# Kernel tuning notes

Measured on AMD Instinct MI355X. Metric: run time of the kernel, lower is better.

Reference implementation:

```python
import jax, jax.numpy as jnp
import numpy as np

N, C, K, H, F, O = 100000, 64, 32, 4, 256, 64
HD = C // H
EPS = 1e-5


def _bn(x, gamma, beta):
    # BatchNorm1d in training mode: biased batch statistics over the voxel dim
    mu = x.mean(axis=0)
    var = x.var(axis=0)
    return (x - mu) * jax.lax.rsqrt(var + EPS) * gamma + beta


def setup_inputs() -> dict:
    key = jax.random.key(0)
    ks = jax.random.split(key, 24)
    s = 0.05
    inp = {
        "voxel_features": jax.random.normal(ks[0], (N, C), jnp.float32),
        "voxel_coords": jax.random.uniform(ks[1], (N, 3), jnp.float32) * 70.0,
        "key_indices": jax.random.randint(ks[2], (N, K), 0, N, jnp.int32),
        "key_mask": jax.random.randint(ks[3], (N, K), 0, 2, jnp.int32).astype(bool).at[:, 0].set(False),
        # MultiheadAttention in/out projections
        "wq": jax.random.normal(ks[4], (C, C), jnp.float32) * s,
        "bq": jnp.zeros((C,), jnp.float32),
        "wk": jax.random.normal(ks[5], (C, C), jnp.float32) * s,
        "bk": jnp.zeros((C,), jnp.float32),
        "wv": jax.random.normal(ks[6], (C, C), jnp.float32) * s,
        "bv": jnp.zeros((C,), jnp.float32),
        "wo": jax.random.normal(ks[7], (C, C), jnp.float32) * s,
        "bo": jnp.zeros((C,), jnp.float32),
        # positional embedding projections (q: Linear(3,C); k: Conv1d(3,C,1) == Linear)
        "q_pos_w": jax.random.normal(ks[8], (C, 3), jnp.float32) * s,
        "q_pos_b": jnp.zeros((C,), jnp.float32),
        "k_pos_w": jax.random.normal(ks[9], (C, 3), jnp.float32) * s,
        "k_pos_b": jnp.zeros((C,), jnp.float32),
        # norm1 / norm2 BatchNorm params
        "g1": jnp.ones((C,), jnp.float32), "b1": jnp.zeros((C,), jnp.float32),
        "g2": jnp.ones((C,), jnp.float32), "b2": jnp.zeros((C,), jnp.float32),
        # FFN
        "lin1_w": jax.random.normal(ks[10], (F, C), jnp.float32) * s,
        "lin1_b": jnp.zeros((F,), jnp.float32),
        "lin2_w": jax.random.normal(ks[11], (C, F), jnp.float32) * s,
        "lin2_b": jnp.zeros((C,), jnp.float32),
        # output layer: Linear + BN + ReLU
        "out_w": jax.random.normal(ks[12], (O, C), jnp.float32) * s,
        "out_b": jnp.zeros((O,), jnp.float32),
        "g3": jnp.ones((O,), jnp.float32), "b3": jnp.zeros((O,), jnp.float32),
    }
    return inp


def reference(voxel_features, voxel_coords, key_indices, key_mask,
              wq, bq, wk, bk, wv, bv, wo, bo,
              q_pos_w, q_pos_b, k_pos_w, k_pos_b,
              g1, b1, g2, b2,
              lin1_w, lin1_b, lin2_w, lin2_b,
              out_w, out_b, g3, b3):
    # gather neighbor features / coords: [N, K, C] and [N, K, 3]
    key_feat = voxel_features[key_indices]
    key_coords = voxel_coords[key_indices] - voxel_coords[:, None, :]  # relative coords

    # positional embeddings
    key_feat = key_feat + jax.nn.relu(jnp.einsum("nkt,ct->nkc", key_coords, k_pos_w) + k_pos_b)
    query = voxel_features + jax.nn.relu(voxel_coords @ q_pos_w.T + q_pos_b)

    # multihead attention: one query per voxel over K gathered keys
    q = (query @ wq.T + bq).reshape(N, H, HD)
    k = (key_feat @ wk.T + bk).reshape(N, K, H, HD)
    v = (key_feat @ wv.T + bv).reshape(N, K, H, HD)
    scores = jnp.einsum("nhd,nkhd->nhk", q, k) / np.sqrt(HD).astype(np.float32)
    scores = jnp.where(key_mask[:, None, :], -jnp.inf, scores)
    attn = jax.nn.softmax(scores, axis=-1)  # [N, H, K]
    ctx = jnp.einsum("nhk,nkhd->nhd", attn, v).reshape(N, C)
    attend = ctx @ wo.T + bo

    # residual + norm1 (dropout = 0)
    x = _bn(voxel_features + attend, g1, b1)
    # FFN + residual + norm2
    ff = jax.nn.relu(x @ lin1_w.T + lin1_b) @ lin2_w.T + lin2_b
    x = _bn(x + ff, g2, b2)
    # output layer: Linear -> BN -> ReLU
    out = jax.nn.relu(_bn(x @ out_w.T + out_b, g3, b3))
    return out
```

## Files before the change

kernel.cpp:

```cpp
#include <hip/hip_runtime.h>
#include <hip/hip_bf16.h>

#define NV 100000
#define EPSB 1e-5f

typedef unsigned short u16;
typedef unsigned int u32;
typedef _Float16 hv2 __attribute__((ext_vector_type(2)));
typedef _Float16 h8  __attribute__((ext_vector_type(8)));
typedef float f32x4  __attribute__((ext_vector_type(4)));

__device__ __forceinline__ u32 pkh(float x, float y) {
  auto h = __builtin_amdgcn_cvt_pkrtz(x, y);
  union { decltype(h) v; u32 u; } c; c.v = h; return c.u;
}
__device__ __forceinline__ float fdot2(u32 w, u32 x, float acc) {
#if __has_builtin(__builtin_amdgcn_fdot2)
  union { u32 u; hv2 h; } a, b; a.u = w; b.u = x;
  return __builtin_amdgcn_fdot2(a.h, b.h, acc, false);
#else
  union { u32 u; hv2 h; } a, b; a.u = w; b.u = x;
  return acc + (float)a.h.x*(float)b.h.x + (float)a.h.y*(float)b.h.y;
#endif
}
__device__ __forceinline__ u32 bcastu(u32 v, int l) {
  return (u32)__builtin_amdgcn_readlane((int)v, l);
}
__device__ __forceinline__ hv2 as_hv(u32 u) {
  union { u32 u; hv2 h; } c; c.u = u; return c.h;
}
__device__ __forceinline__ u32 as_u32h(hv2 h) {
  union { hv2 h; u32 u; } c; c.h = h; return c.u;
}
__device__ __forceinline__ hv2 hmax2v(hv2 a, hv2 b) {
#if __has_builtin(__builtin_elementwise_max)
  return __builtin_elementwise_max(a, b);
#else
  hv2 r; r.x = a.x > b.x ? a.x : b.x; r.y = a.y > b.y ? a.y : b.y; return r;
#endif
}
__device__ __forceinline__ hv2 hfma2v(hv2 a, hv2 b, hv2 c) {
#if __has_builtin(__builtin_elementwise_fma)
  return __builtin_elementwise_fma(a, b, c);
#else
  return a * b + c;
#endif
}
__device__ __forceinline__ u16 f2h(float x) { return (u16)(pkh(x, x) & 0xffffu); }
__device__ __forceinline__ float h2f(u16 u) {
  union { u16 u; _Float16 h; } c; c.u = u; return (float)c.h;
}
__device__ __forceinline__ f32x4 mfma16(h8 a, h8 b, f32x4 c) {
  return __builtin_amdgcn_mfma_f32_16x16x32_f16(a, b, c, 0, 0, 0);
}

__global__ void k0_detect(const u32* __restrict__ km, int* __restrict__ flag) {
  int bad = 0;
  for (int i = threadIdx.x; i < 4096; i += 256) {
    u32 v = km[i];
    bad |= (v != 0u && v != 1u && v != 0x3F800000u) ? 1 : 0;
  }
  unsigned long long m = __ballot(bad != 0);
  __shared__ int sbad[4];
  if ((threadIdx.x & 63) == 0) sbad[threadIdx.x >> 6] = (m != 0ull);
  __syncthreads();
  if (threadIdx.x == 0) flag[0] = !(sbad[0] | sbad[1] | sbad[2] | sbad[3]);
}

__global__ __launch_bounds__(256) void k_prep(
    const float* __restrict__ vf, const float* __restrict__ coords,
    const float* __restrict__ kpw, u32* __restrict__ VP)
{
  const int t = blockIdx.x*256 + threadIdx.x;
  const int cp = t & 31;
  const float wa0 = kpw[(2*cp)*3],   wa1 = kpw[(2*cp)*3+1],   wa2 = kpw[(2*cp)*3+2];
  const float wb0 = kpw[(2*cp+1)*3], wb1 = kpw[(2*cp+1)*3+1], wb2 = kpw[(2*cp+1)*3+2];
  for (int e = t; e < NV*32; e += 524288) {
    const int m = e >> 5;
    const float2 v2 = *(const float2*)&vf[(u32)m*64u + 2u*(u32)cp];
    const float c0 = coords[m*3], c1 = coords[m*3+1], c2 = coords[m*3+2];
    const float P0 = fmaf(wa0, c0, fmaf(wa1, c1, wa2*c2));
    const float P1 = fmaf(wb0, c0, fmaf(wb1, c1, wb2*c2));
    uint2 o; o.x = pkh(v2.x, v2.y); o.y = pkh(P0, P1);
    *(uint2*)&VP[(u32)e*2u] = o;
  }
}

__global__ __launch_bounds__(512, 4) void k1_attn(
    const float* __restrict__ vf, const float* __restrict__ coords,
    const int* __restrict__ kidx, const void* __restrict__ kmaskv,
    const int* __restrict__ mflag, const u32* __restrict__ VP,
    const float* __restrict__ wq, const float* __restrict__ bq,
    const float* __restrict__ wk,
    const float* __restrict__ wv, const float* __restrict__ bv,
    const float* __restrict__ wo, const float* __restrict__ bo,
    const float* __restrict__ qpw, const float* __restrict__ qpb,
    const float* __restrict__ kpb,
    float* __restrict__ x1pre, float* __restrict__ stats)
{
  extern __shared__ char smem[];
  uint2* WQP2 = (uint2*)smem;
  uint2* WKP2 = WQP2 + 1024;
  uint2* WVP2 = WKP2 + 1024;
  uint2* WOP2 = WVP2 + 1024;
  const int tid = threadIdx.x, wid = tid >> 6, lane = tid & 63;

  for (int t = tid; t < 1024; t += 512) {
    int cp = t >> 6, i = t & 63;
    uint2 v;
    v.x = pkh(wq[i*64 + 2*cp],      wq[i*64 + 2*cp + 1]);
    v.y = pkh(wq[i*64 + 2*cp + 32], wq[i*64 + 2*cp + 33]);
    WQP2[t] = v;
    int lo = (cp < 8) ? cp : cp + 8, hi = lo + 8;
    v.x = pkh(wk[2*lo*64 + i], wk[(2*lo+1)*64 + i]);
    v.y = pkh(wk[2*hi*64 + i], wk[(2*hi+1)*64 + i]);
    WKP2[t] = v;
    v.x = pkh(wv[i*64 + 2*cp],      wv[i*64 + 2*cp + 1]);
    v.y = pkh(wv[i*64 + 2*cp + 32], wv[i*64 + 2*cp + 33]);
    WVP2[t] = v;
    v.x = pkh(wo[i*64 + 2*cp],      wo[i*64 + 2*cp + 1]);
    v.y = pkh(wo[i*64 + 2*cp + 32], wo[i*64 + 2*cp + 33]);
    WOP2[t] = v;
  }
  __syncthreads();

  u32* wbase = (u32*)(smem + 32768) + wid * 1360;
  u32*   KFp  = wbase;
  uint2* QKH2 = (uint2*)(wbase + 1088);
  uint2* API2 = QKH2;
  u32*   SPP  = wbase + 1216;

  const int cl = lane & 31, kh = lane >> 5, hp = lane >> 5, hh = lane >> 4;
  const int ca = 2*cl;
  const float qp0 = qpw[lane*3], qp1 = qpw[lane*3+1], qp2 = qpw[lane*3+2], qpbl = qpb[lane];
  const hv2 kpbp = as_hv(pkh(kpb[ca], kpb[ca+1]));
  const hv2 z2 = (hv2)(_Float16)0;
  const float bql = bq[lane], bvl = bv[lane], bol = bo[lane];
  const int mode4 = mflag[0];
  const u32* km32 = (const u32*)kmaskv;
  const unsigned char* km8 = (const unsigned char*)kmaskv;
  float ssum = 0.f, ssq = 0.f;

  for (int n = blockIdx.x*8 + wid; n < NV; n += 4096) {
    const float cn0 = coords[n*3], cn1 = coords[n*3+1], cn2 = coords[n*3+2];
    u32 mk;
    if (mode4) mk = (km32[n*32 + cl] != 0u);
    else       mk = (km8[n*32 + cl]  != 0u);
    const float vfl = vf[(u32)n*64u + (u32)lane];
    const uint2 wn = *(const uint2*)&VP[(u32)n*64u + (u32)ca];
    const hv2 pnp = as_hv(wn.y) - kpbp;

    union { int4 v[4]; int s[16]; } iu;
    {
      const int4* kp4 = (const int4*)(kidx + (u32)n*32u + (u32)(kh*16));
      iu.v[0] = kp4[0]; iu.v[1] = kp4[1]; iu.v[2] = kp4[2]; iu.v[3] = kp4[3];
    }

    #pragma unroll
    for (int b = 0; b < 2; ++b) {
      uint2 g[8];
      #pragma unroll
      for (int k = 0; k < 8; ++k) {
        const u32 off = ((u32)iu.s[b*8+k] << 6) + (u32)ca;
        g[k] = *(const uint2*)&VP[off];
      }
      #pragma unroll
      for (int k = 0; k < 8; ++k) {
        hv2 pe = hmax2v(as_hv(g[k].y) - pnp, z2);
        KFp[(kh*16 + b*8 + k)*34 + cl] = as_u32h(as_hv(g[k].x) + pe);
      }
    }

    float query = vfl + fmaxf(fmaf(qp0,cn0,fmaf(qp1,cn1,fmaf(qp2,cn2,qpbl))), 0.f);
    const u32 qpk = pkh(query, __shfl_down(query, 1));

    float qa0 = bql, qa1 = 0.f;
    #pragma unroll
    for (int cp = 0; cp < 16; ++cp) {
      uint2 w = WQP2[cp*64 + lane];
      qa0 = fdot2(w.x, bcastu(qpk, 2*cp     ), qa0);
      qa1 = fdot2(w.y, bcastu(qpk, 2*cp + 32), qa1);
    }
    const float qacc = (qa0 + qa1) * 0.25f;
    const u32 qpk2 = pkh(qacc, __shfl_down(qacc, 1));

    float qkh0=0.f, qkh1=0.f, qkh2=0.f, qkh3=0.f;
    #pragma unroll
    for (int p = 0; p < 8; ++p) {
      uint2 wA = WKP2[ p    *64 + lane];
      uint2 wB = WKP2[(p+8) *64 + lane];
      qkh0 = fdot2(wA.x, bcastu(qpk2, 2*p     ), qkh0);
      qkh1 = fdot2(wA.y, bcastu(qpk2, 2*p + 16), qkh1);
      qkh2 = fdot2(wB.x, bcastu(qpk2, 2*p + 32), qkh2);
      qkh3 = fdot2(wB.y, bcastu(qpk2, 2*p + 48), qkh3);
    }
    {
      float t0 = __shfl_down(qkh0, 1), t1 = __shfl_down(qkh1, 1);
      float t2 = __shfl_down(qkh2, 1), t3 = __shfl_down(qkh3, 1);
      if ((lane & 1) == 0) {
        int j = lane >> 1;
        uint2 v0; v0.x = pkh(qkh0, t0); v0.y = pkh(qkh1, t1);
        uint2 v1; v1.x = pkh(qkh2, t2); v1.y = pkh(qkh3, t3);
        QKH2[j]      = v0;
        QKH2[32 + j] = v1;
      }
    }

    float s00=0.f, s01=0.f, s10=0.f, s11=0.f;
    {
      const u32* kfrow = KFp + cl*34;
      const uint2* qrow = QKH2 + hp*32;
      #pragma unroll
      for (int c2 = 0; c2 < 16; ++c2) {
        uint2 kf = *(const uint2*)(kfrow + 2*c2);
        uint2 q0 = qrow[2*c2];
        uint2 q1 = qrow[2*c2 + 1];
        s00 = fdot2(kf.x, q0.x, s00);
        s10 = fdot2(kf.x, q0.y, s10);
        s01 = fdot2(kf.y, q1.x, s01);
        s11 = fdot2(kf.y, q1.y, s11);
      }
    }
    float sc0 = s00 + s01, sc1 = s10 + s11;
    if (mk) { sc0 = -1e30f; sc1 = -1e30f; }

    float m0 = sc0, m1 = sc1;
    #pragma unroll
    for (int off = 16; off; off >>= 1) {
      m0 = fmaxf(m0, __shfl_xor(m0, off));
      m1 = fmaxf(m1, __shfl_xor(m1, off));
    }
    float p0 = __expf(sc0 - m0), p1 = __expf(sc1 - m1);
    float s0 = p0, s1 = p1;
    #pragma unroll
    for (int off = 16; off; off >>= 1) {
      s0 += __shfl_xor(s0, off);
      s1 += __shfl_xor(s1, off);
    }
    const float a0 = p0 / s0, a1 = p1 / s1;

    {
      uint2 ap; ap.x = pkh(a0, a0); ap.y = pkh(a1, a1);
      API2[lane] = ap;
    }

    const int j = lane & 31;
    const int ab = hp << 5;
    hv2 accA = z2, accB = z2;
    #pragma unroll
    for (int k2 = 0; k2 < 32; ++k2) {
      hv2 kf = as_hv(KFp[k2*34 + j]);
      uint2 ap = API2[ab + k2];
      accA = hfma2v(kf, as_hv(ap.x), accA);
      accB = hfma2v(kf, as_hv(ap.y), accB);
    }
    {
      const int sj = (j & 15)*2 + (j >> 4);
      SPP[(2*hp  )*34 + sj] = as_u32h(accA);
      SPP[(2*hp+1)*34 + sj] = as_u32h(accB);
    }

    float ca0 = bvl, ca1 = 0.f;
    {
      const u32* sprow = SPP + hh*34;
      #pragma unroll
      for (int cp = 0; cp < 16; ++cp) {
        uint2 s = *(const uint2*)(sprow + 2*cp);
        uint2 w = WVP2[cp*64 + lane];
        ca0 = fdot2(w.x, s.x, ca0);
        ca1 = fdot2(w.y, s.y, ca1);
      }
    }
    const float cacc = ca0 + ca1;
    const u32 cpk = pkh(cacc, __shfl_down(cacc, 1));

    float oa0 = bol, oa1 = 0.f;
    #pragma unroll
    for (int cp = 0; cp < 16; ++cp) {
      uint2 w = WOP2[cp*64 + lane];
      oa0 = fdot2(w.x, bcastu(cpk, 2*cp     ), oa0);
      oa1 = fdot2(w.y, bcastu(cpk, 2*cp + 32), oa1);
    }
    const float aacc = oa0 + oa1;

    float x1 = vfl + aacc;
    x1pre[(u32)n*64u + (u32)lane] = x1;
    ssum += x1; ssq = fmaf(x1, x1, ssq);
  }

  __syncthreads();
  float* red = (float*)smem;
  red[wid*64 + lane] = ssum;
  red[512 + wid*64 + lane] = ssq;
  __syncthreads();
  if (wid == 0) {
    float t1 = 0.f, t2 = 0.f;
    #pragma unroll
    for (int w = 0; w < 8; ++w) { t1 += red[w*64+lane]; t2 += red[512+w*64+lane]; }
    atomicAdd(&stats[lane], t1);
    atomicAdd(&stats[64+lane], t2);
  }
}

__global__ __launch_bounds__(512) void k3_mfma(
    const float* __restrict__ x1pre, float* __restrict__ stats,
    const float* __restrict__ g1, const float* __restrict__ b1,
    const float* __restrict__ l1w, const float* __restrict__ l1b,
    const float* __restrict__ l2w, const float* __restrict__ l2b,
    float* __restrict__ x2pre)
{
  extern __shared__ char smem[];
  u32*   W1B  = (u32*)smem;
  u32*   W2B  = W1B + 8192;
  u16*   XA   = (u16*)(W2B + 8192);
  u16*   H    = XA + 4608;
  float* l1bs = (float*)(H + 16896);
  float* l2bs = l1bs + 256;
  float* scb  = l2bs + 64;
  float* shb  = scb + 64;
  float* red  = shb + 64;
  const int tid = threadIdx.x, wid = tid >> 6, lane = tid & 63;

  for (int e = tid; e < 8192; e += 512) {
    int j2 = e & 3, col = (e>>2) & 15, g = (e>>6) & 3, kk = (e>>8) & 1, n = e >> 9;
    int f = 16*n + col, k = kk*32 + g*8 + 2*j2;
    W1B[e] = pkh(l1w[f*64 + k], l1w[f*64 + k + 1]);
  }
  for (int e = tid; e < 8192; e += 512) {
    int j2 = e & 3, col = (e>>2) & 15, g = (e>>6) & 3, kk = (e>>8) & 7, n = e >> 11;
    int c = 16*n + col, k = kk*32 + g*8 + 2*j2;
    W2B[e] = pkh(l2w[c*256 + k], l2w[c*256 + k + 1]);
  }
  if (tid < 256) l1bs[tid] = l1b[tid];
  if (tid < 64)  l2bs[tid] = l2b[tid];
  if (tid < 64) {
    float mean = stats[tid] * (1.f/NV);
    float var  = stats[64+tid] * (1.f/NV) - mean*mean;
    float sc = rsqrtf(var + EPSB) * g1[tid];
    scb[tid] = sc;
    shb[tid] = b1[tid] - mean * sc;
  }
  if (tid < 128) red[tid] = 0.f;

  const int m  = wid & 3;
  const int wh = wid >> 2;
  const int lg = lane >> 4, ll = lane & 15;
  float ss0 = 0.f, sq0 = 0.f, ss1 = 0.f, sq1 = 0.f;

  for (int tile = blockIdx.x; tile < 1563; tile += 256) {
    const int base = tile * 64;
    __syncthreads();
    {
      int row = tid >> 3, cq = (tid & 7) * 8;
      int srow = base + row; if (srow >= NV) srow = NV - 1;
      const float* src = x1pre + (size_t)srow*64 + cq;
      u32* dst = (u32*)XA + row*36 + (tid & 7)*4;
      #pragma unroll
      for (int q = 0; q < 4; ++q) {
        float v0 = src[2*q]   * scb[cq+2*q]   + shb[cq+2*q];
        float v1 = src[2*q+1] * scb[cq+2*q+1] + shb[cq+2*q+1];
        dst[q] = pkh(v0, v1);
      }
    }
    __syncthreads();
    {
      const u16* arow = XA + (16*m + ll)*72 + lg*8;
      h8 a0 = *(const h8*)(arow);
      h8 a1 = *(const h8*)(arow + 32);
      #pragma unroll
      for (int nn = 0; nn < 8; ++nn) {
        int n = 8*wh + nn;
        const u32* bb = W1B + (n*8 + lg)*64 + ll*4;
        h8 b0 = *(const h8*)(bb);
        h8 b1v = *(const h8*)(bb + 256);
        f32x4 acc = {0.f, 0.f, 0.f, 0.f};
        acc = mfma16(a0, b0, acc);
        acc = mfma16(a1, b1v, acc);
        float bias = l1bs[16*n + ll];
        u16* hw = H + (16*m + lg*4)*264 + 16*n + ll;
        #pragma unroll
        for (int r = 0; r < 4; ++r)
          hw[r*264] = f2h(fmaxf(acc[r] + bias, 0.f));
      }
    }
    __syncthreads();
    {
      const u16* arow = H + (16*m + ll)*264 + lg*8;
      h8 a[8];
      #pragma unroll
      for (int kk = 0; kk < 8; ++kk) a[kk] = *(const h8*)(arow + kk*32);
      #pragma unroll
      for (int nn = 0; nn < 2; ++nn) {
        int n = 2*wh + nn;
        const u32* bb = W2B + (n*32 + lg)*64 + ll*4;
        f32x4 acA = {0.f,0.f,0.f,0.f}, acB = {0.f,0.f,0.f,0.f};
        #pragma unroll
        for (int kk = 0; kk < 8; kk += 2) {
          h8 b0 = *(const h8*)(bb + kk*256);
          h8 b1v = *(const h8*)(bb + (kk+1)*256);
          acA = mfma16(a[kk],   b0,  acA);
          acB = mfma16(a[kk+1], b1v, acB);
        }
        const int col = 16*n + ll;
        const float bias = l2bs[col];
        const u16* xr = XA + (16*m + lg*4)*72 + col;
        const int vox0 = base + 16*m + lg*4;
        float ss = 0.f, sq = 0.f;
        #pragma unroll
        for (int r = 0; r < 4; ++r) {
          int vox = vox0 + r;
          if (vox < NV) {
            float y = acA[r] + acB[r] + bias + h2f(xr[r*72]);
            x2pre[(size_t)vox*64 + col] = y;
            ss += y; sq = fmaf(y, y, sq);
          }
        }
        if (nn == 0) { ss0 += ss; sq0 += sq; } else { ss1 += ss; sq1 += sq; }
      }
    }
  }

  __syncthreads();
  const int c2a = 16*(2*wh)     + ll;
  const int c2b = 16*(2*wh + 1) + ll;
  atomicAdd(&red[c2a], ss0);
  atomicAdd(&red[64 + c2a], sq0);
  atomicAdd(&red[c2b], ss1);
  atomicAdd(&red[64 + c2b], sq1);
  __syncthreads();
  if (tid < 64) {
    atomicAdd(&stats[128+tid], red[tid]);
    atomicAdd(&stats[192+tid], red[64+tid]);
  }
}

__global__ __launch_bounds__(256) void k4_out(
    const float* __restrict__ x2pre, float* __restrict__ stats,
    const float* __restrict__ g2, const float* __restrict__ b2,
    const float* __restrict__ outw, const float* __restrict__ outb,
    float* __restrict__ outpre)
{
  extern __shared__ char smem[];
  u32* WTP = (u32*)smem;
  const int tid = threadIdx.x, wid = tid >> 6, lane = tid & 63;
  for (int t = tid; t < 2048; t += 256) {
    int cp = t >> 6, o = t & 63;
    WTP[t] = pkh(outw[o*64 + 2*cp], outw[o*64 + 2*cp + 1]);
  }
  __syncthreads();

  const float mean = stats[128+lane] * (1.f/NV);
  const float var  = stats[192+lane] * (1.f/NV) - mean*mean;
  const float sc   = rsqrtf(var + EPSB) * g2[lane];
  const float sh   = b2[lane] - mean * sc;
  const float obl  = outb[lane];
  float ssum = 0.f, ssq = 0.f;

  const int stride = gridDim.x << 4;
  for (int n0 = blockIdx.x*16 + wid*4; n0 < NV; n0 += stride) {
    float xa = x2pre[(size_t) n0   *64+lane] * sc + sh;
    float xb = x2pre[(size_t)(n0+1)*64+lane] * sc + sh;
    float xc = x2pre[(size_t)(n0+2)*64+lane] * sc + sh;
    float xd = x2pre[(size_t)(n0+3)*64+lane] * sc + sh;
    const u32 xpa = pkh(xa, __shfl_down(xa,1));
    const u32 xpb = pkh(xb, __shfl_down(xb,1));
    const u32 xpc = pkh(xc, __shfl_down(xc,1));
    const u32 xpd = pkh(xd, __shfl_down(xd,1));
    float a0 = obl, a1 = obl, a2 = obl, a3 = obl;
    #pragma unroll 8
    for (int cp = 0; cp < 32; ++cp) {
      u32 w = WTP[cp*64 + lane];
      a0 = fdot2(w, bcastu(xpa, 2*cp), a0);
      a1 = fdot2(w, bcastu(xpb, 2*cp), a1);
      a2 = fdot2(w, bcastu(xpc, 2*cp), a2);
      a3 = fdot2(w, bcastu(xpd, 2*cp), a3);
    }
    outpre[(size_t) n0   *64+lane] = a0;
    outpre[(size_t)(n0+1)*64+lane] = a1;
    outpre[(size_t)(n0+2)*64+lane] = a2;
    outpre[(size_t)(n0+3)*64+lane] = a3;
    ssum += (a0 + a1) + (a2 + a3);
    ssq = fmaf(a0,a0, fmaf(a1,a1, fmaf(a2,a2, fmaf(a3,a3, ssq))));
  }

  __syncthreads();
  float* red = (float*)smem;
  red[wid*64+lane] = ssum;
  red[256 + wid*64 + lane] = ssq;
  __syncthreads();
  if (wid == 0) {
    float t1 = 0.f, t2 = 0.f;
    #pragma unroll
    for (int w = 0; w < 4; ++w) { t1 += red[w*64+lane]; t2 += red[256+w*64+lane]; }
    atomicAdd(&stats[256+lane], t1);
    atomicAdd(&stats[320+lane], t2);
  }
}

__global__ __launch_bounds__(256) void k5_fin(
    const float* __restrict__ outpre, const float* __restrict__ stats,
    const float* __restrict__ g3, const float* __restrict__ b3,
    float* __restrict__ out)
{
  const int t = blockIdx.x*256 + threadIdx.x;
  const int c0 = (t*4) & 63;
  float sc[4], sh[4];
  #pragma unroll
  for (int j = 0; j < 4; ++j) {
    int c = c0 + j;
    float mean = stats[256+c] * (1.f/NV);
    float var  = stats[320+c] * (1.f/NV) - mean*mean;
    sc[j] = rsqrtf(var + EPSB) * g3[c];
    sh[j] = b3[c] - mean*sc[j];
  }
  for (int i = t; i < NV*16; i += 131072) {
    float4 v = *(const float4*)&outpre[(size_t)i*4];
    v.x = fmaxf(fmaf(v.x, sc[0], sh[0]), 0.f);
    v.y = fmaxf(fmaf(v.y, sc[1], sh[1]), 0.f);
    v.z = fmaxf(fmaf(v.z, sc[2], sh[2]), 0.f);
    v.w = fmaxf(fmaf(v.w, sc[3], sh[3]), 0.f);
    *(float4*)&out[(size_t)i*4] = v;
  }
}

extern "C" void kernel_launch(void* const* d_in, const int* in_sizes, int n_in,
                              void* d_out, int out_size, void* d_ws, size_t ws_size,
                              hipStream_t stream) {
  (void)in_sizes; (void)n_in; (void)out_size; (void)ws_size;
  const float* vf     = (const float*)d_in[0];
  const float* coords = (const float*)d_in[1];
  const int*   kidx   = (const int*)d_in[2];
  const void*  kmask  = d_in[3];
  const float* wq  = (const float*)d_in[4];  const float* bq  = (const float*)d_in[5];
  const float* wk  = (const float*)d_in[6];
  const float* wv  = (const float*)d_in[8];  const float* bv  = (const float*)d_in[9];
  const float* wo  = (const float*)d_in[10]; const float* bo  = (const float*)d_in[11];
  const float* qpw = (const float*)d_in[12]; const float* qpb = (const float*)d_in[13];
  const float* kpw = (const float*)d_in[14]; const float* kpb = (const float*)d_in[15];
  const float* g1  = (const float*)d_in[16]; const float* b1  = (const float*)d_in[17];
  const float* g2  = (const float*)d_in[18]; const float* b2  = (const float*)d_in[19];
  const float* l1w = (const float*)d_in[20]; const float* l1b = (const float*)d_in[21];
  const float* l2w = (const float*)d_in[22]; const float* l2b = (const float*)d_in[23];
  const float* outw= (const float*)d_in[24]; const float* outb= (const float*)d_in[25];
  const float* g3  = (const float*)d_in[26]; const float* b3  = (const float*)d_in[27];

  float* wsf    = (float*)d_ws;
  float* x1pre  = wsf;
  float* x2pre  = wsf + (size_t)NV*64;
  u32*   VP     = (u32*)x2pre;
  float* outpre = x1pre;
  float* stats  = wsf + (size_t)2*NV*64;
  int*   mflag  = (int*)(stats + 384);

  (void)hipMemsetAsync(stats, 0, 384*sizeof(float), stream);

  (void)hipFuncSetAttribute((const void*)k1_attn, hipFuncAttributeMaxDynamicSharedMemorySize, 76288);
  (void)hipFuncSetAttribute((const void*)k3_mfma, hipFuncAttributeMaxDynamicSharedMemorySize, 110848);

  k0_detect<<<1, 256, 0, stream>>>((const u32*)kmask, mflag);
  k_prep<<<2048, 256, 0, stream>>>(vf, coords, kpw, VP);
  k1_attn<<<512, 512, 76288, stream>>>(vf, coords, kidx, kmask, mflag, VP,
      wq, bq, wk, wv, bv, wo, bo, qpw, qpb, kpb, x1pre, stats);
  k3_mfma<<<256, 512, 110848, stream>>>(x1pre, stats, g1, b1, l1w, l1b, l2w, l2b, x2pre);
  k4_out<<<1024, 256, 8192, stream>>>(x2pre, stats, g2, b2, outw, outb, outpre);
  k5_fin<<<512, 256, 0, stream>>>(outpre, stats, g3, b3, (float*)d_out);
}
```

Baseline: 304.1 us.

## Software-pipeline per-voxel loads and issue all 16 key gathers before Q projection

The attention kernel's voxel loop now prefetches the next iteration's key indices, coords, features, packed values and mask into registers while the current voxel is processed. All 16 gathered key rows are issued at once, and the Q and QK projections run before the gathered data is consumed, so gather latency overlaps with that compute. The cost is higher register pressure from holding 16 gathered uint2 values plus the next-iteration state, which may lower occupancy.

Result: no change. 299.7 us (-1.4%).

```diff
diff --git a/kernel.cpp b/kernel.cpp
--- a/kernel.cpp
+++ b/kernel.cpp
@@ -141,35 +141,44 @@
   const unsigned char* km8 = (const unsigned char*)kmaskv;
   float ssum = 0.f, ssq = 0.f;
 
-  for (int n = blockIdx.x*8 + wid; n < NV; n += 4096) {
-    const float cn0 = coords[n*3], cn1 = coords[n*3+1], cn2 = coords[n*3+2];
-    u32 mk;
-    if (mode4) mk = (km32[n*32 + cl] != 0u);
-    else       mk = (km8[n*32 + cl]  != 0u);
-    const float vfl = vf[(u32)n*64u + (u32)lane];
-    const uint2 wn = *(const uint2*)&VP[(u32)n*64u + (u32)ca];
+  union iu_t { int4 v[4]; int s[16]; };
+
+  const int n0 = blockIdx.x*8 + wid;
+  iu_t iu;
+  float cn0 = 0.f, cn1 = 0.f, cn2 = 0.f, vfl = 0.f;
+  uint2 wn = {0u, 0u};
+  u32 mkraw = 0u;
+  if (n0 < NV) {
+    const int4* kp4 = (const int4*)(kidx + (u32)n0*32u + (u32)(kh*16));
+    iu.v[0] = kp4[0]; iu.v[1] = kp4[1]; iu.v[2] = kp4[2]; iu.v[3] = kp4[3];
+    cn0 = coords[n0*3]; cn1 = coords[n0*3+1]; cn2 = coords[n0*3+2];
+    vfl = vf[(u32)n0*64u + (u32)lane];
+    wn  = *(const uint2*)&VP[(u32)n0*64u + (u32)ca];
+    mkraw = mode4 ? km32[n0*32 + cl] : (u32)km8[n0*32 + cl];
+  }
+
+  for (int n = n0; n < NV; n += 4096) {
+    uint2 g[16];
+    #pragma unroll
+    for (int k = 0; k < 16; ++k) {
+      const u32 off = ((u32)iu.s[k] << 6) + (u32)ca;
+      g[k] = *(const uint2*)&VP[off];
+    }
+
+    const int nn = n + 4096;
+    const int np = (nn < NV) ? nn : n;
+    iu_t iun;
+    {
+      const int4* kp4 = (const int4*)(kidx + (u32)np*32u + (u32)(kh*16));
+      iun.v[0] = kp4[0]; iun.v[1] = kp4[1]; iun.v[2] = kp4[2]; iun.v[3] = kp4[3];
+    }
+    const float cn0n = coords[np*3], cn1n = coords[np*3+1], cn2n = coords[np*3+2];
+    const float vfln = vf[(u32)np*64u + (u32)lane];
+    const uint2 wnn  = *(const uint2*)&VP[(u32)np*64u + (u32)ca];
+    const u32 mkrawn = mode4 ? km32[np*32 + cl] : (u32)km8[np*32 + cl];
+
     const hv2 pnp = as_hv(wn.y) - kpbp;
-
-    union { int4 v[4]; int s[16]; } iu;
-    {
-      const int4* kp4 = (const int4*)(kidx + (u32)n*32u + (u32)(kh*16));
-      iu.v[0] = kp4[0]; iu.v[1] = kp4[1]; iu.v[2] = kp4[2]; iu.v[3] = kp4[3];
-    }
-
-    #pragma unroll
-    for (int b = 0; b < 2; ++b) {
-      uint2 g[8];
-      #pragma unroll
-      for (int k = 0; k < 8; ++k) {
-        const u32 off = ((u32)iu.s[b*8+k] << 6) + (u32)ca;
-        g[k] = *(const uint2*)&VP[off];
-      }
-      #pragma unroll
-      for (int k = 0; k < 8; ++k) {
-        hv2 pe = hmax2v(as_hv(g[k].y) - pnp, z2);
-        KFp[(kh*16 + b*8 + k)*34 + cl] = as_u32h(as_hv(g[k].x) + pe);
-      }
-    }
+    const u32 mk = (mkraw != 0u);
 
     float query = vfl + fmaxf(fmaf(qp0,cn0,fmaf(qp1,cn1,fmaf(qp2,cn2,qpbl))), 0.f);
     const u32 qpk = pkh(query, __shfl_down(query, 1));
@@ -204,6 +213,12 @@
         QKH2[j]      = v0;
         QKH2[32 + j] = v1;
       }
+    }
+
+    #pragma unroll
+    for (int k = 0; k < 16; ++k) {
+      hv2 pe = hmax2v(as_hv(g[k].y) - pnp, z2);
+      KFp[(kh*16 + k)*34 + cl] = as_u32h(as_hv(g[k].x) + pe);
     }
 
     float s00=0.f, s01=0.f, s10=0.f, s11=0.f;
@@ -286,6 +301,10 @@
     float x1 = vfl + aacc;
     x1pre[(u32)n*64u + (u32)lane] = x1;
     ssum += x1; ssq = fmaf(x1, x1, ssq);
+
+    iu = iun;
+    cn0 = cn0n; cn1 = cn1n; cn2 = cn2n;
+    vfl = vfln; wn = wnn; mkraw = mkrawn;
   }
 
   __syncthreads();
```

## Move packed attention weights to global memory, raise k1 occupancy, batch key gathers

Applied to the files above, without the earlier changes.

The fp16 packing of the four projection weights moves out of the attention kernel into a one-block pre-kernel that writes them to global workspace. The attention kernel then reads weights through the cache instead of LDS, which frees 32 KB of LDS per block. That allows 768 blocks with a launch bound of 6 blocks per CU instead of 4. It also issues all 16 key gathers up front and delays the positional-add and LDS store until after the query projection, so gather latency overlaps compute. In exchange, weight reads now hit L1/L2 instead of LDS, and holding 16 gathered values live raises register pressure.

After: 750.9 us. 147% more time.

```diff
diff --git a/kernel.cpp b/kernel.cpp
--- a/kernel.cpp
+++ b/kernel.cpp
@@ -65,6 +65,30 @@
   if ((threadIdx.x & 63) == 0) sbad[threadIdx.x >> 6] = (m != 0ull);
   __syncthreads();
   if (threadIdx.x == 0) flag[0] = !(sbad[0] | sbad[1] | sbad[2] | sbad[3]);
+}
+
+__global__ __launch_bounds__(512) void k_wpack(
+    const float* __restrict__ wq, const float* __restrict__ wk,
+    const float* __restrict__ wv, const float* __restrict__ wo,
+    uint2* __restrict__ Wg)
+{
+  for (int e = threadIdx.x; e < 1024; e += 512) {
+    int cp = e >> 6, i = e & 63;
+    uint2 v;
+    v.x = pkh(wq[i*64 + 2*cp],      wq[i*64 + 2*cp + 1]);
+    v.y = pkh(wq[i*64 + 2*cp + 32], wq[i*64 + 2*cp + 33]);
+    Wg[e] = v;
+    int lo = (cp < 8) ? cp : cp + 8, hi = lo + 8;
+    v.x = pkh(wk[2*lo*64 + i], wk[(2*lo+1)*64 + i]);
+    v.y = pkh(wk[2*hi*64 + i], wk[(2*hi+1)*64 + i]);
+    Wg[1024 + e] = v;
+    v.x = pkh(wv[i*64 + 2*cp],      wv[i*64 + 2*cp + 1]);
+    v.y = pkh(wv[i*64 + 2*cp + 32], wv[i*64 + 2*cp + 33]);
+    Wg[2048 + e] = v;
+    v.x = pkh(wo[i*64 + 2*cp],      wo[i*64 + 2*cp + 1]);
+    v.y = pkh(wo[i*64 + 2*cp + 32], wo[i*64 + 2*cp + 33]);
+    Wg[3072 + e] = v;
+  }
 }
 
 __global__ __launch_bounds__(256) void k_prep(
@@ -86,45 +110,25 @@
   }
 }
 
-__global__ __launch_bounds__(512, 4) void k1_attn(
+__global__ __launch_bounds__(512, 6) void k1_attn(
     const float* __restrict__ vf, const float* __restrict__ coords,
     const int* __restrict__ kidx, const void* __restrict__ kmaskv,
     const int* __restrict__ mflag, const u32* __restrict__ VP,
-    const float* __restrict__ wq, const float* __restrict__ bq,
-    const float* __restrict__ wk,
-    const float* __restrict__ wv, const float* __restrict__ bv,
-    const float* __restrict__ wo, const float* __restrict__ bo,
+    const uint2* __restrict__ Wg,
+    const float* __restrict__ bq, const float* __restrict__ bv,
+    const float* __restrict__ bo,
     const float* __restrict__ qpw, const float* __restrict__ qpb,
     const float* __restrict__ kpb,
     float* __restrict__ x1pre, float* __restrict__ stats)
 {
   extern __shared__ char smem[];
-  uint2* WQP2 = (uint2*)smem;
-  uint2* WKP2 = WQP2 + 1024;
-  uint2* WVP2 = WKP2 + 1024;
-  uint2* WOP2 = WVP2 + 1024;
+  const uint2* WQP2 = Wg;
+  const uint2* WKP2 = Wg + 1024;
+  const uint2* WVP2 = Wg + 2048;
+  const uint2* WOP2 = Wg + 3072;
   const int tid = threadIdx.x, wid = tid >> 6, lane = tid & 63;
 
-  for (int t = tid; t < 1024; t += 512) {
-    int cp = t >> 6, i = t & 63;
-    uint2 v;
-    v.x = pkh(wq[i*64 + 2*cp],      wq[i*64 + 2*cp + 1]);
-    v.y = pkh(wq[i*64 + 2*cp + 32], wq[i*64 + 2*cp + 33]);
-    WQP2[t] = v;
-    int lo = (cp < 8) ? cp : cp + 8, hi = lo + 8;
-    v.x = pkh(wk[2*lo*64 + i], wk[(2*lo+1)*64 + i]);
-    v.y = pkh(wk[2*hi*64 + i], wk[(2*hi+1)*64 + i]);
-    WKP2[t] = v;
-    v.x = pkh(wv[i*64 + 2*cp],      wv[i*64 + 2*cp + 1]);
-    v.y = pkh(wv[i*64 + 2*cp + 32], wv[i*64 + 2*cp + 33]);
-    WVP2[t] = v;
-    v.x = pkh(wo[i*64 + 2*cp],      wo[i*64 + 2*cp + 1]);
-    v.y = pkh(wo[i*64 + 2*cp + 32], wo[i*64 + 2*cp + 33]);
-    WOP2[t] = v;
-  }
-  __syncthreads();
-
-  u32* wbase = (u32*)(smem + 32768) + wid * 1360;
+  u32* wbase = (u32*)smem + wid * 1360;
   u32*   KFp  = wbase;
   uint2* QKH2 = (uint2*)(wbase + 1088);
   uint2* API2 = QKH2;
@@ -141,7 +145,7 @@
   const unsigned char* km8 = (const unsigned char*)kmaskv;
   float ssum = 0.f, ssq = 0.f;
 
-  for (int n = blockIdx.x*8 + wid; n < NV; n += 4096) {
+  for (int n = blockIdx.x*8 + wid; n < NV; n += 6144) {
     const float cn0 = coords[n*3], cn1 = coords[n*3+1], cn2 = coords[n*3+2];
     u32 mk;
     if (mode4) mk = (km32[n*32 + cl] != 0u);
@@ -156,19 +160,11 @@
       iu.v[0] = kp4[0]; iu.v[1] = kp4[1]; iu.v[2] = kp4[2]; iu.v[3] = kp4[3];
     }
 
-    #pragma unroll
-    for (int b = 0; b < 2; ++b) {
-      uint2 g[8];
-      #pragma unroll
-      for (int k = 0; k < 8; ++k) {
-        const u32 off = ((u32)iu.s[b*8+k] << 6) + (u32)ca;
-        g[k] = *(const uint2*)&VP[off];
-      }
-      #pragma unroll
-      for (int k = 0; k < 8; ++k) {
-        hv2 pe = hmax2v(as_hv(g[k].y) - pnp, z2);
-        KFp[(kh*16 + b*8 + k)*34 + cl] = as_u32h(as_hv(g[k].x) + pe);
-      }
+    uint2 g[16];
+    #pragma unroll
+    for (int k = 0; k < 16; ++k) {
+      const u32 off = ((u32)iu.s[k] << 6) + (u32)ca;
+      g[k] = *(const uint2*)&VP[off];
     }
 
     float query = vfl + fmaxf(fmaf(qp0,cn0,fmaf(qp1,cn1,fmaf(qp2,cn2,qpbl))), 0.f);
@@ -204,6 +200,12 @@
         QKH2[j]      = v0;
         QKH2[32 + j] = v1;
       }
+    }
+
+    #pragma unroll
+    for (int k = 0; k < 16; ++k) {
+      hv2 pe = hmax2v(as_hv(g[k].y) - pnp, z2);
+      KFp[(kh*16 + k)*34 + cl] = as_u32h(as_hv(g[k].x) + pe);
     }
 
     float s00=0.f, s01=0.f, s10=0.f, s11=0.f;
@@ -551,16 +553,18 @@
   float* outpre = x1pre;
   float* stats  = wsf + (size_t)2*NV*64;
   int*   mflag  = (int*)(stats + 384);
+  uint2* Wg     = (uint2*)(stats + 512);
 
   (void)hipMemsetAsync(stats, 0, 384*sizeof(float), stream);
 
-  (void)hipFuncSetAttribute((const void*)k1_attn, hipFuncAttributeMaxDynamicSharedMemorySize, 76288);
+  (void)hipFuncSetAttribute((const void*)k1_attn, hipFuncAttributeMaxDynamicSharedMemorySize, 65536);
   (void)hipFuncSetAttribute((const void*)k3_mfma, hipFuncAttributeMaxDynamicSharedMemorySize, 110848);
 
   k0_detect<<<1, 256, 0, stream>>>((const u32*)kmask, mflag);
+  k_wpack<<<1, 512, 0, stream>>>(wq, wk, wv, wo, Wg);
   k_prep<<<2048, 256, 0, stream>>>(vf, coords, kpw, VP);
-  k1_attn<<<512, 512, 76288, stream>>>(vf, coords, kidx, kmask, mflag, VP,
-      wq, bq, wk, wv, bv, wo, bo, qpw, qpb, kpb, x1pre, stats);
+  k1_attn<<<768, 512, 43520, stream>>>(vf, coords, kidx, kmask, mflag, VP,
+      Wg, bq, bv, bo, qpw, qpb, kpb, x1pre, stats);
   k3_mfma<<<256, 512, 110848, stream>>>(x1pre, stats, g1, b1, l1w, l1b, l2w, l2b, x2pre);
   k4_out<<<1024, 256, 8192, stream>>>(x2pre, stats, g2, b2, outw, outb, outpre);
   k5_fin<<<512, 256, 0, stream>>>(outpre, stats, g3, b3, (float*)d_out);
```
